# Optimization experiments

Measured on AMD Instinct MI355X. Metric: run time of the kernel, lower is better.

Reference implementation:

```python
import jax, jax.numpy as jnp
import numpy as np

B, S, D, H = 4, 1024, 1024, 16
DH = D // H
K_SPARSE = 32
LAMBDA_MAX, ALPHA = 10.0, 5.0
SPARSE_THRESHOLD = 1.0


def setup_inputs() -> dict:
    key = jax.random.key(0)
    ks = jax.random.split(key, 12)
    x = jax.random.normal(ks[0], (B, S, D), dtype=jnp.float32)
    prior_mask = jax.random.bernoulli(ks[1], 0.1, (S, S))
    prior_indices = jax.random.randint(ks[2], (S, K_SPARSE), 0, S)
    prior_index_mask = jax.random.bernoulli(ks[3], 0.9, (S, K_SPARSE))
    prior_index_mask = prior_index_mask.at[:, 0].set(True)  # avoid all-masked rows
    u_prev = jax.random.normal(ks[4], (B, 1), dtype=jnp.float32)
    sc = 1.0 / np.sqrt(D)
    Wq = jax.random.normal(ks[5], (D, D), dtype=jnp.float32) * sc
    Wk = jax.random.normal(ks[6], (D, D), dtype=jnp.float32) * sc
    Wv = jax.random.normal(ks[7], (D, D), dtype=jnp.float32) * sc
    Wo = jax.random.normal(ks[8], (D, D), dtype=jnp.float32) * sc
    bq = jnp.zeros((D,), jnp.float32)
    bk = jnp.zeros((D,), jnp.float32)
    bv = jnp.zeros((D,), jnp.float32)
    bo = jnp.zeros((D,), jnp.float32)
    return {"x": x, "prior_mask": prior_mask, "prior_indices": prior_indices,
            "prior_index_mask": prior_index_mask, "u_prev": u_prev,
            "Wq": Wq, "bq": bq, "Wk": Wk, "bk": bk, "Wv": Wv, "bv": bv,
            "Wo": Wo, "bo": bo}


def reference(x, prior_mask, prior_indices, prior_index_mask, u_prev,
              Wq, bq, Wk, bk, Wv, bv, Wo, bo):
    Bb, Ss, Dd = x.shape
    scale = 1.0 / jnp.sqrt(jnp.asarray(DH, x.dtype))

    def proj(W, b):
        return (x @ W.T + b).reshape(Bb, Ss, H, DH).transpose(0, 2, 1, 3)  # [B,H,S,DH]

    Q, K, V = proj(Wq, bq), proj(Wk, bk), proj(Wv, bv)

    lam = LAMBDA_MAX * jnp.exp(-ALPHA * u_prev.reshape(Bb))  # [B]
    use_sparse = lam >= SPARSE_THRESHOLD                      # [B] bool

    # ---- dense branch: full SDPA with lambda-scaled prior bias ----
    scores = jnp.einsum('bhqd,bhkd->bhqk', Q, K) * scale      # [B,H,S,S]
    prior_bias = jnp.where(prior_mask[:Ss, :Ss], 0.0, -1.0).astype(x.dtype)
    bias = lam[:, None, None, None] * prior_bias[None, None]
    dense_out = jnp.einsum('bhqk,bhkd->bhqd',
                           jax.nn.softmax(scores + bias, axis=-1), V)

    # ---- sparse branch: gather-indexed SDPA over prior_indices ----
    idx = prior_indices[:Ss]                                   # [S,k]
    Kg = K[:, :, idx]                                          # [B,H,S,k,DH]
    Vg = V[:, :, idx]
    s_scores = jnp.einsum('bhsd,bhskd->bhsk', Q, Kg) * scale   # [B,H,S,k]
    s_scores = jnp.where(prior_index_mask[:Ss][None, None], s_scores,
                         jnp.asarray(-jnp.inf, x.dtype))
    sparse_out = jnp.einsum('bhsk,bhskd->bhsd',
                            jax.nn.softmax(s_scores, axis=-1), Vg)

    out = jnp.where(use_sparse[:, None, None, None], sparse_out, dense_out)
    out = out.transpose(0, 2, 1, 3).reshape(Bb, Ss, Dd)
    return out @ Wo.T + bo
```

## Files before the change

### kernel.cpp

```cpp
#include <hip/hip_runtime.h>
#include <hip/hip_bf16.h>
#include <cmath>

#define NB 4
#define NS 1024
#define ND 1024
#define NH 16
#define NDH 64
#define NKSP 32
#define SCALE 0.125f
#define LOG2E 1.44269504f
#define SCALE2 (SCALE * LOG2E)

typedef __attribute__((ext_vector_type(8))) short bf16x8;
typedef __attribute__((ext_vector_type(4))) float f32x4;
typedef unsigned long long u64;

#define AS1 __attribute__((address_space(1)))
#define AS3 __attribute__((address_space(3)))

__device__ __forceinline__ void gl_lds16(const void* g, void* l) {
    __builtin_amdgcn_global_load_lds((const AS1 void*)g, (AS3 void*)l, 16, 0, 0);
}

__device__ __forceinline__ ushort f2bf(float f) {
    union { __hip_bfloat16 h; ushort u; } cv;
    cv.h = __float2bfloat16(f);
    return cv.u;
}
__device__ __forceinline__ float bf2f(ushort u) {
    union { unsigned int i; float f; } cv;
    cv.i = ((unsigned int)u) << 16;
    return cv.f;
}
__device__ __forceinline__ float fexp2(float x) {
    return __builtin_amdgcn_exp2f(x);
}

__global__ __launch_bounds__(256)
void f2bf_multi(const float* __restrict__ x,
                const float* __restrict__ w0, const float* __restrict__ w1,
                const float* __restrict__ w2, const float* __restrict__ w3,
                const int* __restrict__ pm,
                ushort* __restrict__ xo,
                ushort* __restrict__ o0, ushort* __restrict__ o1,
                ushort* __restrict__ o2, ushort* __restrict__ o3,
                u64* __restrict__ bm)
{
    int y = blockIdx.y;
    if (y == 5) {
        int word = blockIdx.x * 4 + (threadIdx.x >> 6);
        int lane = threadIdx.x & 63;
        int row  = word >> 4, wcol = word & 15;
        int v = pm[(size_t)row * NS + wcol * 64 + lane];
        u64 b = __ballot(v != 0);
        if (lane == 0) bm[word] = b;
        return;
    }
    const float* src; ushort* dst; int nblk;
    if (y == 0)      { src = x;  dst = xo; nblk = 4096; }
    else if (y == 1) { src = w0; dst = o0; nblk = 1024; }
    else if (y == 2) { src = w1; dst = o1; nblk = 1024; }
    else if (y == 3) { src = w2; dst = o2; nblk = 1024; }
    else             { src = w3; dst = o3; nblk = 1024; }
    if (blockIdx.x >= (unsigned)nblk) return;
    int i = (blockIdx.x * 256 + threadIdx.x) * 4;
    float4 v = *(const float4*)&src[i];
    ushort4 o;
    o.x = f2bf(v.x); o.y = f2bf(v.y); o.z = f2bf(v.z); o.w = f2bf(v.w);
    *(ushort4*)&dst[i] = o;
}

__global__ __launch_bounds__(256)
void gemm_qkv(const ushort* __restrict__ xb,
              const ushort* __restrict__ Wqb, const ushort* __restrict__ Wkb,
              const ushort* __restrict__ Wvb,
              const float* __restrict__ bq, const float* __restrict__ bk,
              const float* __restrict__ bv,
              ushort* __restrict__ Qo, ushort* __restrict__ Ko,
              ushort* __restrict__ Vo, ushort* __restrict__ Vto)
{
    constexpr int K = ND;
    __shared__ __attribute__((aligned(16))) ushort As[128 * 32];
    __shared__ __attribute__((aligned(16))) ushort Bs[128 * 32];

    const int tid  = threadIdx.x;
    const int lane = tid & 63, w = tid >> 6;
    const int wm = w >> 1, wn = w & 1;
    const int which = blockIdx.x >> 3;
    const int n0 = (blockIdx.x & 7) * 128;
    const int m0 = blockIdx.y * 128;
    const int quad = lane >> 4, l16 = lane & 15;

    const ushort* W = (which == 0) ? Wqb : (which == 1) ? Wkb : Wvb;
    const float* bias = (which == 0) ? bq : (which == 1) ? bk : bv;
    ushort* Out = (which == 0) ? Qo : (which == 1) ? Ko : Vo;

    f32x4 acc[4][4] = {};

    for (int k0 = 0; k0 < K; k0 += 32) {
        __syncthreads();
#pragma unroll
        for (int u = 0; u < 2; ++u) {
            int t0 = u * 256 + w * 64;
            int t  = t0 + lane;
            int row = t >> 2, kc = (t & 3) * 8;
            gl_lds16(xb + (size_t)(m0 + row) * K + k0 + kc, &As[t0 * 8]);
            gl_lds16(W  + (size_t)(n0 + row) * K + k0 + kc, &Bs[t0 * 8]);
        }
        __syncthreads();

        bf16x8 af[4], bfr[4];
#pragma unroll
        for (int mt = 0; mt < 4; ++mt)
            af[mt] = *(const bf16x8*)&As[(wm*64 + mt*16 + l16) * 32 + quad*8];
#pragma unroll
        for (int nt = 0; nt < 4; ++nt)
            bfr[nt] = *(const bf16x8*)&Bs[(wn*64 + nt*16 + l16) * 32 + quad*8];
#pragma unroll
        for (int mt = 0; mt < 4; ++mt)
#pragma unroll
            for (int nt = 0; nt < 4; ++nt)
                acc[mt][nt] = __builtin_amdgcn_mfma_f32_16x16x32_bf16(
                    af[mt], bfr[nt], acc[mt][nt], 0, 0, 0);
    }

#pragma unroll
    for (int nt = 0; nt < 4; ++nt) {
        int n = n0 + wn*64 + nt*16 + l16;
        float bz = bias[n];
        int hh = n >> 6, dh = n & 63;
#pragma unroll
        for (int mt = 0; mt < 4; ++mt) {
#pragma unroll
            for (int rg = 0; rg < 4; ++rg) {
                int m = m0 + wm*64 + mt*16 + quad*4 + rg;
                int b = m >> 10, s = m & (NS - 1);
                ushort val = f2bf(acc[mt][nt][rg] + bz);
                Out[(((size_t)(b*NH + hh))*NS + s)*NDH + dh] = val;
                if (which == 2)
                    Vto[(((size_t)(b*NH + hh))*NDH + dh)*NS + s] = val;
            }
        }
    }
}

__global__ __launch_bounds__(256)
void gemm_out(const ushort* __restrict__ A, const ushort* __restrict__ W,
              const float* __restrict__ bias, float* __restrict__ Cout)
{
    constexpr int K = ND;
    __shared__ __attribute__((aligned(16))) ushort As[64 * 32];
    __shared__ __attribute__((aligned(16))) ushort Bs[128 * 32];

    const int tid  = threadIdx.x;
    const int lane = tid & 63, w = tid >> 6;
    const int wm = w & 1, wn = w >> 1;
    const int m0 = blockIdx.y * 64, n0 = blockIdx.x * 128;
    const int quad = lane >> 4, l16 = lane & 15;

    f32x4 acc[2][4] = {};

    for (int k0 = 0; k0 < K; k0 += 32) {
        __syncthreads();
        {
            int t0 = w * 64;
            int t  = t0 + lane;
            int row = t >> 2, kc = (t & 3) * 8;
            gl_lds16(A + (size_t)(m0 + row) * K + k0 + kc, &As[t0 * 8]);
        }
#pragma unroll
        for (int u = 0; u < 2; ++u) {
            int t0 = u * 256 + w * 64;
            int t  = t0 + lane;
            int row = t >> 2, kc = (t & 3) * 8;
            gl_lds16(W + (size_t)(n0 + row) * K + k0 + kc, &Bs[t0 * 8]);
        }
        __syncthreads();

        bf16x8 af[2], bfr[4];
#pragma unroll
        for (int mt = 0; mt < 2; ++mt)
            af[mt] = *(const bf16x8*)&As[(wm*32 + mt*16 + l16) * 32 + quad*8];
#pragma unroll
        for (int nt = 0; nt < 4; ++nt)
            bfr[nt] = *(const bf16x8*)&Bs[(wn*64 + nt*16 + l16) * 32 + quad*8];
#pragma unroll
        for (int mt = 0; mt < 2; ++mt)
#pragma unroll
            for (int nt = 0; nt < 4; ++nt)
                acc[mt][nt] = __builtin_amdgcn_mfma_f32_16x16x32_bf16(
                    af[mt], bfr[nt], acc[mt][nt], 0, 0, 0);
    }

#pragma unroll
    for (int nt = 0; nt < 4; ++nt) {
        int n = n0 + wn*64 + nt*16 + l16;
        float bz = bias[n];
#pragma unroll
        for (int mt = 0; mt < 2; ++mt) {
#pragma unroll
            for (int rg = 0; rg < 4; ++rg) {
                int m = m0 + wm*32 + mt*16 + quad*4 + rg;
                Cout[(size_t)m * ND + n] = acc[mt][nt][rg] + bz;
            }
        }
    }
}


#define STAGE(T4)                                                             \
    _Pragma("unroll")                                                         \
    for (int u = 0; u < 4; ++u) {                                             \
        int cb = w * 256 + u * 64;                                            \
        int c  = cb + lane;                                                   \
        int tk = c >> 9, c2 = c & 511;                                        \
        int row = c2 >> 3, sub = c2 & 7;                                      \
        const ushort* src = Kh + (((size_t)(((T4)*4 + tk)*64 + row)) << 6)    \
                               + ((sub ^ (row & 7)) << 3);                    \
        gl_lds16(src, KK + (size_t)cb * 8);                                   \
    }

#define LOADKV(KF, VF, KT)                                                    \
    _Pragma("unroll")                                                         \
    for (int nt = 0; nt < 4; ++nt)                                            \
        _Pragma("unroll")                                                     \
        for (int kk = 0; kk < 2; ++kk) {                                      \
            int rowk = nt*16 + l16;                                           \
            int ck = (kk*4 + quad) ^ (l16 & 7);                               \
            KF[nt][kk] = *(const bf16x8*)&KK[wk*4096 + rowk*64 + ck*8];       \
            VF[nt][kk] = *(const bf16x8*)                                     \
                &Vth[(size_t)(nt*16 + l16) * NS + (KT)*64 + kk*32 + quad*8];  \
        }

#define STEP(KF, VF, M0, M1)                                                  \
    _Pragma("unroll")                                                         \
    for (int qh = 0; qh < 2; ++qh) {                                          \
        const int qrow = wq*32 + qh*16 + l16;                                 \
        u64 wqm = ((qh == 0) ? (M0) : (M1)) >> (quad * 4);                    \
        f32x4 s_acc[4] = {};                                                  \
        __builtin_amdgcn_s_setprio(1);                                        \
        _Pragma("unroll")                                                     \
        for (int nt = 0; nt < 4; ++nt)                                        \
            _Pragma("unroll")                                                 \
            for (int kk = 0; kk < 2; ++kk)                                    \
                s_acc[nt] = __builtin_amdgcn_mfma_f32_16x16x32_bf16(          \
                    KF[nt][kk], qf[qh][kk], s_acc[nt], 0, 0, 0);              \
        __builtin_amdgcn_s_setprio(0);                                        \
        _Pragma("unroll")                                                     \
        for (int nt = 0; nt < 4; ++nt) {                                      \
            ushort4 pk;                                                       \
            float p0 = fexp2(fmaf(s_acc[nt][0], SCALE2,                       \
                 ((wqm >> (nt*16 + 0)) & 1ULL) ? 0.f : nlam2));               \
            float p1 = fexp2(fmaf(s_acc[nt][1], SCALE2,                       \
                 ((wqm >> (nt*16 + 1)) & 1ULL) ? 0.f : nlam2));               \
            float p2 = fexp2(fmaf(s_acc[nt][2], SCALE2,                       \
                 ((wqm >> (nt*16 + 2)) & 1ULL) ? 0.f : nlam2));               \
            float p3 = fexp2(fmaf(s_acc[nt][3], SCALE2,                       \
                 ((wqm >> (nt*16 + 3)) & 1ULL) ? 0.f : nlam2));               \
            pk.x = f2bf(p0); pk.y = f2bf(p1);                                 \
            pk.z = f2bf(p2); pk.w = f2bf(p3);                                 \
            *(ushort4*)&Ps[wk*4608 + qrow*72 + nt*16 + quad*4] = pk;          \
        }                                                                     \
        bf16x8 pf[2];                                                         \
        _Pragma("unroll")                                                     \
        for (int kk = 0; kk < 2; ++kk)                                        \
            pf[kk] = *(const bf16x8*)&Ps[wk*4608 + qrow*72 + kk*32 + quad*8]; \
        __builtin_amdgcn_s_setprio(1);                                        \
        _Pragma("unroll")                                                     \
        for (int kk = 0; kk < 2; ++kk) {                                      \
            l_acc[qh] = __builtin_amdgcn_mfma_f32_16x16x32_bf16(              \
                pf[kk], ones.v, l_acc[qh], 0, 0, 0);                          \
            _Pragma("unroll")                                                 \
            for (int nt = 0; nt < 4; ++nt)                                    \
                o_acc[qh][nt] = __builtin_amdgcn_mfma_f32_16x16x32_bf16(      \
                    pf[kk], VF[nt][kk], o_acc[qh][nt], 0, 0, 0);              \
        }                                                                     \
        __builtin_amdgcn_s_setprio(0);                                        \
    }

__global__ __launch_bounds__(512)
void attn_kernel(const ushort* __restrict__ Qb, const ushort* __restrict__ Kb,
                 const ushort* __restrict__ Vb, const ushort* __restrict__ Vt,
                 const u64* __restrict__ bm,
                 const int* __restrict__ pidx, const int* __restrict__ pimask,
                 const float* __restrict__ u_prev, ushort* __restrict__ OA)
{
    __shared__ __attribute__((aligned(16))) ushort SM[34816];
    ushort* KK = SM;
    ushort* Ps = SM + 16384;

    const int tid  = threadIdx.x;
    const int lane = tid & 63, w = tid >> 6;
    const int quad = lane >> 4, l16 = lane & 15;
    const int wq = w & 1, wk = w >> 1;

    float lams[4];
#pragma unroll
    for (int i = 0; i < 4; ++i) lams[i] = 10.0f * __expf(-5.0f * u_prev[i]);
    int dl[4], sl[4], nd = 0, ns = 0;
#pragma unroll
    for (int i = 0; i < 4; ++i) if (lams[i] <  1.0f) dl[nd++] = i;
#pragma unroll
    for (int i = 0; i < 4; ++i) if (lams[i] >= 1.0f) sl[ns++] = i;

    const int id = blockIdx.x;
    bool sparse; int b, h, qtile;
    if (id < nd * 256) {
        sparse = false;
        int xcd = id & 7, j = id >> 3;
        int nh2 = 2 * nd;
        int hi = j % nh2, qt = j / nh2;
        int gh = hi * 8 + xcd;
        b = dl[gh >> 4]; h = gh & 15; qtile = qt;
    } else {
        sparse = true;
        int d = id - nd * 256;
        int xcd = d & 7, j = d >> 3;
        int nh2 = 2 * ns;
        int hi = j % nh2, qt = j / nh2;
        int gh = hi * 8 + xcd;
        b = sl[gh >> 4]; h = gh & 15; qtile = qt;
    }
    const int s0 = qtile * 64;
    const float lam = lams[b];

    const size_t bh = (size_t)b * NH + h;
    const ushort* Qh  = Qb + bh * NS * NDH;
    const ushort* Kh  = Kb + bh * NS * NDH;
    const ushort* Vh  = Vb + bh * NS * NDH;
    const ushort* Vth = Vt + bh * NDH * NS;

    if (!sparse) {
        const float nlam2 = -lam * LOG2E;

        bf16x8 qf[2][2];
#pragma unroll
        for (int qh = 0; qh < 2; ++qh)
#pragma unroll
            for (int kk = 0; kk < 2; ++kk)
                qf[qh][kk] = *(const bf16x8*)
                    &Qh[(size_t)(s0 + wq*32 + qh*16 + l16) * NDH + kk*32 + quad*8];

        union { bf16x8 v; ushort s[8]; } ones;
#pragma unroll
        for (int i = 0; i < 8; ++i) ones.s[i] = 0x3F80;

        f32x4 o_acc[2][4] = {};
        f32x4 l_acc[2] = {};

        for (int t = 0; t < 4; ++t) {
            if (t) __syncthreads();
            STAGE(t);
            const int kt = 4 * t + wk;
            u64 m0 = bm[(size_t)(s0 + wq*32 +  0 + l16) * 16 + kt];
            u64 m1 = bm[(size_t)(s0 + wq*32 + 16 + l16) * 16 + kt];
            __syncthreads();
            bf16x8 kf[4][2], vf[4][2];
            LOADKV(kf, vf, kt);
            STEP(kf, vf, m0, m1);
        }
        __syncthreads();

        float* POUT = (float*)SM;
        if (wk != 0) {
            int base = ((wk - 1) * 2 + wq) * 2560;
#pragma unroll
            for (int qh = 0; qh < 2; ++qh) {
#pragma unroll
                for (int nt = 0; nt < 4; ++nt)
#pragma unroll
                    for (int rg = 0; rg < 4; ++rg)
                        POUT[base + (qh*16 + nt*4 + rg)*64 + lane] =
                            o_acc[qh][nt][rg];
#pragma unroll
                for (int rg = 0; rg < 4; ++rg)
                    POUT[base + (32 + qh*4 + rg)*64 + lane] = l_acc[qh][rg];
            }
        }
        __syncthreads();
        if (wk == 0) {
#pragma unroll
            for (int s = 0; s < 3; ++s) {
                int base = (s * 2 + wq) * 2560;
#pragma unroll
                for (int qh = 0; qh < 2; ++qh) {
#pragma unroll
                    for (int nt = 0; nt < 4; ++nt)
#pragma unroll
                        for (int rg = 0; rg < 4; ++rg)
                            o_acc[qh][nt][rg] +=
                                POUT[base + (qh*16 + nt*4 + rg)*64 + lane];
#pragma unroll
                    for (int rg = 0; rg < 4; ++rg)
                        l_acc[qh][rg] += POUT[base + (32 + qh*4 + rg)*64 + lane];
                }
            }
#pragma unroll
            for (int qh = 0; qh < 2; ++qh) {
                float inv[4];
#pragma unroll
                for (int rg = 0; rg < 4; ++rg) inv[rg] = 1.f / l_acc[qh][rg];
#pragma unroll
                for (int nt = 0; nt < 4; ++nt)
#pragma unroll
                    for (int rg = 0; rg < 4; ++rg) {
                        int m = wq*32 + qh*16 + quad*4 + rg;
                        OA[((size_t)b*NS + s0 + m)*ND + h*NDH + nt*16 + l16] =
                            f2bf(o_acc[qh][nt][rg] * inv[rg]);
                    }
            }
        }
    } else {
        if (w >= 4) return;
        const int r2  = lane & 15;
        const int cg  = lane >> 4;
        {
            const int row = w*16 + r2;

            float qreg[64];
            {
                const ushort* qp = Qh + (size_t)(s0 + row) * NDH;
#pragma unroll
                for (int c = 0; c < 8; ++c) {
                    union { bf16x8 v; ushort s[8]; } qv;
                    qv.v = *(const bf16x8*)(qp + c*8);
#pragma unroll
                    for (int j = 0; j < 8; ++j) qreg[c*8 + j] = bf2f(qv.s[j]);
                }
            }

            float sc[8];
#pragma unroll
            for (int jj = 0; jj < 8; ++jj) {
                int j  = cg*8 + jj;
                int mv = pimask[(size_t)(s0+row)*NKSP + j];
                int kv = pidx[(size_t)(s0+row)*NKSP + j];
                const ushort* krow = &Kh[(size_t)kv * NDH];
                float acc = 0.f;
#pragma unroll
                for (int c = 0; c < 8; ++c) {
                    union { bf16x8 v; ushort s[8]; } kk;
                    kk.v = *(const bf16x8*)(krow + c*8);
#pragma unroll
                    for (int jb = 0; jb < 8; ++jb)
                        acc = fmaf(qreg[c*8 + jb], bf2f(kk.s[jb]), acc);
                }
                sc[jj] = mv ? acc * SCALE : -INFINITY;
            }
            float mt = sc[0];
#pragma unroll
            for (int jj = 1; jj < 8; ++jj) mt = fmaxf(mt, sc[jj]);
            mt = fmaxf(mt, __shfl_xor(mt, 16));
            mt = fmaxf(mt, __shfl_xor(mt, 32));

            float psum = 0.f;
#pragma unroll
            for (int jj = 0; jj < 8; ++jj) {
                float p = __expf(sc[jj] - mt);
                psum += p;
                Ps[row * 72 + cg*8 + jj] = f2bf(p);
            }
            psum += __shfl_xor(psum, 16);
            psum += __shfl_xor(psum, 32);

            float o[16];
#pragma unroll
            for (int i = 0; i < 16; ++i) o[i] = 0.f;

#pragma unroll 4
            for (int j = 0; j < 32; ++j) {
                float p = bf2f(Ps[row * 72 + j]);
                int kv = pidx[(size_t)(s0+row)*NKSP + j];
                const ushort* vrow = &Vh[(size_t)kv * NDH + cg*16];
#pragma unroll
                for (int c = 0; c < 2; ++c) {
                    union { bf16x8 v; ushort s[8]; } vv;
                    vv.v = *(const bf16x8*)(vrow + c*8);
#pragma unroll
                    for (int jb = 0; jb < 8; ++jb)
                        o[c*8 + jb] = fmaf(p, bf2f(vv.s[jb]), o[c*8 + jb]);
                }
            }

            float inv = 1.f / psum;
            ushort* op = OA + ((size_t)b*NS + s0 + row)*ND + h*NDH + cg*16;
#pragma unroll
            for (int i4 = 0; i4 < 4; ++i4) {
                ushort4 v;
                v.x = f2bf(o[i4*4+0]*inv); v.y = f2bf(o[i4*4+1]*inv);
                v.z = f2bf(o[i4*4+2]*inv); v.w = f2bf(o[i4*4+3]*inv);
                *(ushort4*)(op + i4*4) = v;
            }
        }
    }
}

extern "C" void kernel_launch(void* const* d_in, const int* in_sizes, int n_in,
                              void* d_out, int out_size, void* d_ws, size_t ws_size,
                              hipStream_t stream)
{
    const float* x      = (const float*)d_in[0];
    const int*   pmask  = (const int*)  d_in[1];
    const int*   pidx   = (const int*)  d_in[2];
    const int*   pimask = (const int*)  d_in[3];
    const float* u_prev = (const float*)d_in[4];
    const float* Wq     = (const float*)d_in[5];
    const float* bq     = (const float*)d_in[6];
    const float* Wk     = (const float*)d_in[7];
    const float* bk     = (const float*)d_in[8];
    const float* Wv     = (const float*)d_in[9];
    const float* bv     = (const float*)d_in[10];
    const float* Wo     = (const float*)d_in[11];
    const float* bo     = (const float*)d_in[12];
    float* out = (float*)d_out;

    const size_t QSZ = (size_t)NB * NH * NS * NDH;
    const size_t WSZ = (size_t)ND * ND;
    ushort* xb  = (ushort*)d_ws;
    ushort* Qw  = xb  + QSZ;
    ushort* Kw  = Qw  + QSZ;
    ushort* Vw  = Kw  + QSZ;
    ushort* Vtw = Vw  + QSZ;
    ushort* Awb = Vtw + QSZ;
    ushort* Wqb = Awb + QSZ;
    ushort* Wkb = Wqb + WSZ;
    ushort* Wvb = Wkb + WSZ;
    ushort* Wob = Wvb + WSZ;
    u64*    bmw = (u64*)(Wob + WSZ);

    f2bf_multi<<<dim3(4096, 6), 256, 0, stream>>>(
        x, Wq, Wk, Wv, Wo, pmask, xb, Wqb, Wkb, Wvb, Wob, bmw);

    gemm_qkv<<<dim3(24, 32), 256, 0, stream>>>(
        xb, Wqb, Wkb, Wvb, bq, bk, bv, Qw, Kw, Vw, Vtw);

    attn_kernel<<<1024, 512, 0, stream>>>(
        Qw, Kw, Vw, Vtw, bmw, pidx, pimask, u_prev, Awb);

    gemm_out<<<dim3(ND/128, (NB*NS)/64), 256, 0, stream>>>(Awb, Wob, bo, out);
}
```

Before: 236.2 us.

## Split attention into separate dense and sparse kernels with smaller blocks

Replaces the single 512-thread attention kernel with two launches: a 256-thread dense kernel covering 32 query rows per block and a 256-thread sparse kernel. The old sparse path wasted half its block because four warps exited immediately, and dense blocks carried 512 threads with large LDS. Smaller dense tiles double the block count and should improve occupancy, at the cost of each block staging the same 64 KV rows for half as many queries, plus one extra kernel launch.

```diff
diff --git a/kernel.cpp b/kernel.cpp
--- a/kernel.cpp
+++ b/kernel.cpp
@@ -209,10 +209,10 @@
 }
 
 
-#define STAGE(T4)                                                             \
+#define DSTAGE(T4)                                                            \
     _Pragma("unroll")                                                         \
-    for (int u = 0; u < 4; ++u) {                                             \
-        int cb = w * 256 + u * 64;                                            \
+    for (int u = 0; u < 8; ++u) {                                             \
+        int cb = w * 512 + u * 64;                                            \
         int c  = cb + lane;                                                   \
         int tk = c >> 9, c2 = c & 511;                                        \
         int row = c2 >> 3, sub = c2 & 7;                                      \
@@ -221,22 +221,22 @@
         gl_lds16(src, KK + (size_t)cb * 8);                                   \
     }
 
-#define LOADKV(KF, VF, KT)                                                    \
+#define DLOADKV(KF, VF, KT)                                                   \
     _Pragma("unroll")                                                         \
     for (int nt = 0; nt < 4; ++nt)                                            \
         _Pragma("unroll")                                                     \
         for (int kk = 0; kk < 2; ++kk) {                                      \
             int rowk = nt*16 + l16;                                           \
             int ck = (kk*4 + quad) ^ (l16 & 7);                               \
-            KF[nt][kk] = *(const bf16x8*)&KK[wk*4096 + rowk*64 + ck*8];       \
+            KF[nt][kk] = *(const bf16x8*)&KK[w*4096 + rowk*64 + ck*8];        \
             VF[nt][kk] = *(const bf16x8*)                                     \
                 &Vth[(size_t)(nt*16 + l16) * NS + (KT)*64 + kk*32 + quad*8];  \
         }
 
-#define STEP(KF, VF, M0, M1)                                                  \
+#define DSTEP(KF, VF, M0, M1)                                                 \
     _Pragma("unroll")                                                         \
     for (int qh = 0; qh < 2; ++qh) {                                          \
-        const int qrow = wq*32 + qh*16 + l16;                                 \
+        const int qrow = qh*16 + l16;                                         \
         u64 wqm = ((qh == 0) ? (M0) : (M1)) >> (quad * 4);                    \
         f32x4 s_acc[4] = {};                                                  \
         __builtin_amdgcn_s_setprio(1);                                        \
@@ -260,12 +260,12 @@
                  ((wqm >> (nt*16 + 3)) & 1ULL) ? 0.f : nlam2));               \
             pk.x = f2bf(p0); pk.y = f2bf(p1);                                 \
             pk.z = f2bf(p2); pk.w = f2bf(p3);                                 \
-            *(ushort4*)&Ps[wk*4608 + qrow*72 + nt*16 + quad*4] = pk;          \
+            *(ushort4*)&Ps[w*2304 + qrow*72 + nt*16 + quad*4] = pk;           \
         }                                                                     \
         bf16x8 pf[2];                                                         \
         _Pragma("unroll")                                                     \
         for (int kk = 0; kk < 2; ++kk)                                        \
-            pf[kk] = *(const bf16x8*)&Ps[wk*4608 + qrow*72 + kk*32 + quad*8]; \
+            pf[kk] = *(const bf16x8*)&Ps[w*2304 + qrow*72 + kk*32 + quad*8];  \
         __builtin_amdgcn_s_setprio(1);                                        \
         _Pragma("unroll")                                                     \
         for (int kk = 0; kk < 2; ++kk) {                                      \
@@ -279,220 +279,231 @@
         __builtin_amdgcn_s_setprio(0);                                        \
     }
 
-__global__ __launch_bounds__(512)
-void attn_kernel(const ushort* __restrict__ Qb, const ushort* __restrict__ Kb,
-                 const ushort* __restrict__ Vb, const ushort* __restrict__ Vt,
-                 const u64* __restrict__ bm,
+__global__ __launch_bounds__(256)
+void attn_dense(const ushort* __restrict__ Qb, const ushort* __restrict__ Kb,
+                const ushort* __restrict__ Vt, const u64* __restrict__ bm,
+                const float* __restrict__ u_prev, ushort* __restrict__ OA)
+{
+    __shared__ __attribute__((aligned(16))) ushort SM[25600];
+    ushort* KK = SM;
+    ushort* Ps = SM + 16384;
+
+    const int tid  = threadIdx.x;
+    const int lane = tid & 63, w = tid >> 6;
+    const int quad = lane >> 4, l16 = lane & 15;
+
+    float lams[4];
+#pragma unroll
+    for (int i = 0; i < 4; ++i) lams[i] = 10.0f * __expf(-5.0f * u_prev[i]);
+    int dl[4], nd = 0;
+#pragma unroll
+    for (int i = 0; i < 4; ++i) if (lams[i] < 1.0f) dl[nd++] = i;
+
+    const int id = blockIdx.x;
+    if (id >= nd * 512) return;
+
+    int xcd = id & 7, j = id >> 3;
+    int nh2 = 2 * nd;
+    int hi = j % nh2, qt = j / nh2;
+    int gh = hi * 8 + xcd;
+    const int b = dl[gh >> 4], h = gh & 15;
+    const int s0 = qt * 32;
+    const float nlam2 = -lams[b] * LOG2E;
+
+    const size_t bh = (size_t)b * NH + h;
+    const ushort* Qh  = Qb + bh * NS * NDH;
+    const ushort* Kh  = Kb + bh * NS * NDH;
+    const ushort* Vth = Vt + bh * NDH * NS;
+
+    bf16x8 qf[2][2];
+#pragma unroll
+    for (int qh = 0; qh < 2; ++qh)
+#pragma unroll
+        for (int kk = 0; kk < 2; ++kk)
+            qf[qh][kk] = *(const bf16x8*)
+                &Qh[(size_t)(s0 + qh*16 + l16) * NDH + kk*32 + quad*8];
+
+    union { bf16x8 v; ushort s[8]; } ones;
+#pragma unroll
+    for (int i = 0; i < 8; ++i) ones.s[i] = 0x3F80;
+
+    f32x4 o_acc[2][4] = {};
+    f32x4 l_acc[2] = {};
+
+    for (int t = 0; t < 4; ++t) {
+        if (t) __syncthreads();
+        DSTAGE(t);
+        const int kt = 4 * t + w;
+        u64 m0 = bm[(size_t)(s0 +  0 + l16) * 16 + kt];
+        u64 m1 = bm[(size_t)(s0 + 16 + l16) * 16 + kt];
+        __syncthreads();
+        bf16x8 kf[4][2], vf[4][2];
+        DLOADKV(kf, vf, kt);
+        DSTEP(kf, vf, m0, m1);
+    }
+    __syncthreads();
+
+    float* POUT = (float*)SM;
+    if (w != 0) {
+        int base = (w - 1) * 2560;
+#pragma unroll
+        for (int qh = 0; qh < 2; ++qh) {
+#pragma unroll
+            for (int nt = 0; nt < 4; ++nt)
+#pragma unroll
+                for (int rg = 0; rg < 4; ++rg)
+                    POUT[base + (qh*16 + nt*4 + rg)*64 + lane] =
+                        o_acc[qh][nt][rg];
+#pragma unroll
+            for (int rg = 0; rg < 4; ++rg)
+                POUT[base + (32 + qh*4 + rg)*64 + lane] = l_acc[qh][rg];
+        }
+    }
+    __syncthreads();
+    if (w == 0) {
+#pragma unroll
+        for (int s = 0; s < 3; ++s) {
+            int base = s * 2560;
+#pragma unroll
+            for (int qh = 0; qh < 2; ++qh) {
+#pragma unroll
+                for (int nt = 0; nt < 4; ++nt)
+#pragma unroll
+                    for (int rg = 0; rg < 4; ++rg)
+                        o_acc[qh][nt][rg] +=
+                            POUT[base + (qh*16 + nt*4 + rg)*64 + lane];
+#pragma unroll
+                for (int rg = 0; rg < 4; ++rg)
+                    l_acc[qh][rg] += POUT[base + (32 + qh*4 + rg)*64 + lane];
+            }
+        }
+#pragma unroll
+        for (int qh = 0; qh < 2; ++qh) {
+            float inv[4];
+#pragma unroll
+            for (int rg = 0; rg < 4; ++rg) inv[rg] = 1.f / l_acc[qh][rg];
+#pragma unroll
+            for (int nt = 0; nt < 4; ++nt)
+#pragma unroll
+                for (int rg = 0; rg < 4; ++rg) {
+                    int m = qh*16 + quad*4 + rg;
+                    OA[((size_t)b*NS + s0 + m)*ND + h*NDH + nt*16 + l16] =
+                        f2bf(o_acc[qh][nt][rg] * inv[rg]);
+                }
+        }
+    }
+}
+
+__global__ __launch_bounds__(256)
+void attn_sparse(const ushort* __restrict__ Qb, const ushort* __restrict__ Kb,
+                 const ushort* __restrict__ Vb,
                  const int* __restrict__ pidx, const int* __restrict__ pimask,
                  const float* __restrict__ u_prev, ushort* __restrict__ OA)
 {
-    __shared__ __attribute__((aligned(16))) ushort SM[34816];
-    ushort* KK = SM;
-    ushort* Ps = SM + 16384;
+    __shared__ __attribute__((aligned(16))) ushort Ps[64 * 72];
 
     const int tid  = threadIdx.x;
     const int lane = tid & 63, w = tid >> 6;
-    const int quad = lane >> 4, l16 = lane & 15;
-    const int wq = w & 1, wk = w >> 1;
 
     float lams[4];
 #pragma unroll
     for (int i = 0; i < 4; ++i) lams[i] = 10.0f * __expf(-5.0f * u_prev[i]);
-    int dl[4], sl[4], nd = 0, ns = 0;
-#pragma unroll
-    for (int i = 0; i < 4; ++i) if (lams[i] <  1.0f) dl[nd++] = i;
+    int sl[4], ns = 0;
 #pragma unroll
     for (int i = 0; i < 4; ++i) if (lams[i] >= 1.0f) sl[ns++] = i;
 
     const int id = blockIdx.x;
-    bool sparse; int b, h, qtile;
-    if (id < nd * 256) {
-        sparse = false;
-        int xcd = id & 7, j = id >> 3;
-        int nh2 = 2 * nd;
-        int hi = j % nh2, qt = j / nh2;
-        int gh = hi * 8 + xcd;
-        b = dl[gh >> 4]; h = gh & 15; qtile = qt;
-    } else {
-        sparse = true;
-        int d = id - nd * 256;
-        int xcd = d & 7, j = d >> 3;
-        int nh2 = 2 * ns;
-        int hi = j % nh2, qt = j / nh2;
-        int gh = hi * 8 + xcd;
-        b = sl[gh >> 4]; h = gh & 15; qtile = qt;
-    }
-    const int s0 = qtile * 64;
-    const float lam = lams[b];
+    if (id >= ns * 256) return;
+
+    int xcd = id & 7, j = id >> 3;
+    int nh2 = 2 * ns;
+    int hi = j % nh2, qt = j / nh2;
+    int gh = hi * 8 + xcd;
+    const int b = sl[gh >> 4], h = gh & 15;
+    const int s0 = qt * 64;
 
     const size_t bh = (size_t)b * NH + h;
-    const ushort* Qh  = Qb + bh * NS * NDH;
-    const ushort* Kh  = Kb + bh * NS * NDH;
-    const ushort* Vh  = Vb + bh * NS * NDH;
-    const ushort* Vth = Vt + bh * NDH * NS;
-
-    if (!sparse) {
-        const float nlam2 = -lam * LOG2E;
-
-        bf16x8 qf[2][2];
-#pragma unroll
-        for (int qh = 0; qh < 2; ++qh)
-#pragma unroll
-            for (int kk = 0; kk < 2; ++kk)
-                qf[qh][kk] = *(const bf16x8*)
-                    &Qh[(size_t)(s0 + wq*32 + qh*16 + l16) * NDH + kk*32 + quad*8];
-
-        union { bf16x8 v; ushort s[8]; } ones;
-#pragma unroll
-        for (int i = 0; i < 8; ++i) ones.s[i] = 0x3F80;
-
-        f32x4 o_acc[2][4] = {};
-        f32x4 l_acc[2] = {};
-
-        for (int t = 0; t < 4; ++t) {
-            if (t) __syncthreads();
-            STAGE(t);
-            const int kt = 4 * t + wk;
-            u64 m0 = bm[(size_t)(s0 + wq*32 +  0 + l16) * 16 + kt];
-            u64 m1 = bm[(size_t)(s0 + wq*32 + 16 + l16) * 16 + kt];
-            __syncthreads();
-            bf16x8 kf[4][2], vf[4][2];
-            LOADKV(kf, vf, kt);
-            STEP(kf, vf, m0, m1);
-        }
-        __syncthreads();
-
-        float* POUT = (float*)SM;
-        if (wk != 0) {
-            int base = ((wk - 1) * 2 + wq) * 2560;
-#pragma unroll
-            for (int qh = 0; qh < 2; ++qh) {
-#pragma unroll
-                for (int nt = 0; nt < 4; ++nt)
-#pragma unroll
-                    for (int rg = 0; rg < 4; ++rg)
-                        POUT[base + (qh*16 + nt*4 + rg)*64 + lane] =
-                            o_acc[qh][nt][rg];
-#pragma unroll
-                for (int rg = 0; rg < 4; ++rg)
-                    POUT[base + (32 + qh*4 + rg)*64 + lane] = l_acc[qh][rg];
-            }
-        }
-        __syncthreads();
-        if (wk == 0) {
-#pragma unroll
-            for (int s = 0; s < 3; ++s) {
-                int base = (s * 2 + wq) * 2560;
-#pragma unroll
-                for (int qh = 0; qh < 2; ++qh) {
-#pragma unroll
-                    for (int nt = 0; nt < 4; ++nt)
-#pragma unroll
-                        for (int rg = 0; rg < 4; ++rg)
-                            o_acc[qh][nt][rg] +=
-                                POUT[base + (qh*16 + nt*4 + rg)*64 + lane];
-#pragma unroll
-                    for (int rg = 0; rg < 4; ++rg)
-                        l_acc[qh][rg] += POUT[base + (32 + qh*4 + rg)*64 + lane];
-                }
-            }
-#pragma unroll
-            for (int qh = 0; qh < 2; ++qh) {
-                float inv[4];
-#pragma unroll
-                for (int rg = 0; rg < 4; ++rg) inv[rg] = 1.f / l_acc[qh][rg];
-#pragma unroll
-                for (int nt = 0; nt < 4; ++nt)
-#pragma unroll
-                    for (int rg = 0; rg < 4; ++rg) {
-                        int m = wq*32 + qh*16 + quad*4 + rg;
-                        OA[((size_t)b*NS + s0 + m)*ND + h*NDH + nt*16 + l16] =
-                            f2bf(o_acc[qh][nt][rg] * inv[rg]);
-                    }
-            }
-        }
-    } else {
-        if (w >= 4) return;
-        const int r2  = lane & 15;
-        const int cg  = lane >> 4;
-        {
-            const int row = w*16 + r2;
-
-            float qreg[64];
-            {
-                const ushort* qp = Qh + (size_t)(s0 + row) * NDH;
-#pragma unroll
-                for (int c = 0; c < 8; ++c) {
-                    union { bf16x8 v; ushort s[8]; } qv;
-                    qv.v = *(const bf16x8*)(qp + c*8);
-#pragma unroll
-                    for (int j = 0; j < 8; ++j) qreg[c*8 + j] = bf2f(qv.s[j]);
-                }
-            }
-
-            float sc[8];
-#pragma unroll
-            for (int jj = 0; jj < 8; ++jj) {
-                int j  = cg*8 + jj;
-                int mv = pimask[(size_t)(s0+row)*NKSP + j];
-                int kv = pidx[(size_t)(s0+row)*NKSP + j];
-                const ushort* krow = &Kh[(size_t)kv * NDH];
-                float acc = 0.f;
-#pragma unroll
-                for (int c = 0; c < 8; ++c) {
-                    union { bf16x8 v; ushort s[8]; } kk;
-                    kk.v = *(const bf16x8*)(krow + c*8);
-#pragma unroll
-                    for (int jb = 0; jb < 8; ++jb)
-                        acc = fmaf(qreg[c*8 + jb], bf2f(kk.s[jb]), acc);
-                }
-                sc[jj] = mv ? acc * SCALE : -INFINITY;
-            }
-            float mt = sc[0];
-#pragma unroll
-            for (int jj = 1; jj < 8; ++jj) mt = fmaxf(mt, sc[jj]);
-            mt = fmaxf(mt, __shfl_xor(mt, 16));
-            mt = fmaxf(mt, __shfl_xor(mt, 32));
-
-            float psum = 0.f;
-#pragma unroll
-            for (int jj = 0; jj < 8; ++jj) {
-                float p = __expf(sc[jj] - mt);
-                psum += p;
-                Ps[row * 72 + cg*8 + jj] = f2bf(p);
-            }
-            psum += __shfl_xor(psum, 16);
-            psum += __shfl_xor(psum, 32);
-
-            float o[16];
-#pragma unroll
-            for (int i = 0; i < 16; ++i) o[i] = 0.f;
+    const ushort* Qh = Qb + bh * NS * NDH;
+    const ushort* Kh = Kb + bh * NS * NDH;
+    const ushort* Vh = Vb + bh * NS * NDH;
+
+    const int r2 = lane & 15;
+    const int cg = lane >> 4;
+    const int row = w*16 + r2;
+
+    float qreg[64];
+    {
+        const ushort* qp = Qh + (size_t)(s0 + row) * NDH;
+#pragma unroll
+        for (int c = 0; c < 8; ++c) {
+            union { bf16x8 v; ushort s[8]; } qv;
+            qv.v = *(const bf16x8*)(qp + c*8);
+#pragma unroll
+            for (int jj = 0; jj < 8; ++jj) qreg[c*8 + jj] = bf2f(qv.s[jj]);
+        }
+    }
+
+    float sc[8];
+#pragma unroll
+    for (int jj = 0; jj < 8; ++jj) {
+        int jx = cg*8 + jj;
+        int mv = pimask[(size_t)(s0+row)*NKSP + jx];
+        int kv = pidx[(size_t)(s0+row)*NKSP + jx];
+        const ushort* krow = &Kh[(size_t)kv * NDH];
+        float acc = 0.f;
+#pragma unroll
+        for (int c = 0; c < 8; ++c) {
+            union { bf16x8 v; ushort s[8]; } kk;
+            kk.v = *(const bf16x8*)(krow + c*8);
+#pragma unroll
+            for (int jb = 0; jb < 8; ++jb)
+                acc = fmaf(qreg[c*8 + jb], bf2f(kk.s[jb]), acc);
+        }
+        sc[jj] = mv ? acc * SCALE : -INFINITY;
+    }
+    float mt = sc[0];
+#pragma unroll
+    for (int jj = 1; jj < 8; ++jj) mt = fmaxf(mt, sc[jj]);
+    mt = fmaxf(mt, __shfl_xor(mt, 16));
+    mt = fmaxf(mt, __shfl_xor(mt, 32));
+
+    float psum = 0.f;
+#pragma unroll
+    for (int jj = 0; jj < 8; ++jj) {
+        float p = __expf(sc[jj] - mt);
+        psum += p;
+        Ps[row * 72 + cg*8 + jj] = f2bf(p);
+    }
+    psum += __shfl_xor(psum, 16);
+    psum += __shfl_xor(psum, 32);
+
+    float o[16];
+#pragma unroll
+    for (int i = 0; i < 16; ++i) o[i] = 0.f;
 
 #pragma unroll 4
-            for (int j = 0; j < 32; ++j) {
-                float p = bf2f(Ps[row * 72 + j]);
-                int kv = pidx[(size_t)(s0+row)*NKSP + j];
-                const ushort* vrow = &Vh[(size_t)kv * NDH + cg*16];
-#pragma unroll
-                for (int c = 0; c < 2; ++c) {
-                    union { bf16x8 v; ushort s[8]; } vv;
-                    vv.v = *(const bf16x8*)(vrow + c*8);
-#pragma unroll
-                    for (int jb = 0; jb < 8; ++jb)
-                        o[c*8 + jb] = fmaf(p, bf2f(vv.s[jb]), o[c*8 + jb]);
-                }
-            }
-
-            float inv = 1.f / psum;
-            ushort* op = OA + ((size_t)b*NS + s0 + row)*ND + h*NDH + cg*16;
-#pragma unroll
-            for (int i4 = 0; i4 < 4; ++i4) {
-                ushort4 v;
-                v.x = f2bf(o[i4*4+0]*inv); v.y = f2bf(o[i4*4+1]*inv);
-                v.z = f2bf(o[i4*4+2]*inv); v.w = f2bf(o[i4*4+3]*inv);
-                *(ushort4*)(op + i4*4) = v;
-            }
-        }
+    for (int jx = 0; jx < 32; ++jx) {
+        float p = bf2f(Ps[row * 72 + jx]);
+        int kv = pidx[(size_t)(s0+row)*NKSP + jx];
+        const ushort* vrow = &Vh[(size_t)kv * NDH + cg*16];
+#pragma unroll
+        for (int c = 0; c < 2; ++c) {
+            union { bf16x8 v; ushort s[8]; } vv;
+            vv.v = *(const bf16x8*)(vrow + c*8);
+#pragma unroll
+            for (int jb = 0; jb < 8; ++jb)
+                o[c*8 + jb] = fmaf(p, bf2f(vv.s[jb]), o[c*8 + jb]);
+        }
+    }
+
+    float inv = 1.f / psum;
+    ushort* op = OA + ((size_t)b*NS + s0 + row)*ND + h*NDH + cg*16;
+#pragma unroll
+    for (int i4 = 0; i4 < 4; ++i4) {
+        ushort4 v;
+        v.x = f2bf(o[i4*4+0]*inv); v.y = f2bf(o[i4*4+1]*inv);
+        v.z = f2bf(o[i4*4+2]*inv); v.w = f2bf(o[i4*4+3]*inv);
+        *(ushort4*)(op + i4*4) = v;
     }
 }
 
@@ -535,8 +546,11 @@
     gemm_qkv<<<dim3(24, 32), 256, 0, stream>>>(
         xb, Wqb, Wkb, Wvb, bq, bk, bv, Qw, Kw, Vw, Vtw);
 
-    attn_kernel<<<1024, 512, 0, stream>>>(
-        Qw, Kw, Vw, Vtw, bmw, pidx, pimask, u_prev, Awb);
+    attn_dense<<<2048, 256, 0, stream>>>(
+        Qw, Kw, Vtw, bmw, u_prev, Awb);
+
+    attn_sparse<<<1024, 256, 0, stream>>>(
+        Qw, Kw, Vw, pidx, pimask, u_prev, Awb);
 
     gemm_out<<<dim3(ND/128, (NB*NS)/64), 256, 0, stream>>>(Awb, Wob, bo, out);
 }
```

Result: slower. 253.0 us (+7.1%).
